# Kernel optimization log

Measured on AMD Instinct MI355X. Metric: run time of the kernel, lower is better.

Reference implementation:

```python
import jax, jax.numpy as jnp
import numpy as np

LN_EPS = 1e-5


def _ln(x, g, b):
    m = jnp.mean(x, axis=-1, keepdims=True)
    v = jnp.mean((x - m) ** 2, axis=-1, keepdims=True)
    return (x - m) / jnp.sqrt(v + LN_EPS) * g + b


def setup_inputs() -> dict:
    key = jax.random.key(0)
    ks = jax.random.split(key, 8)
    B, N, S, D, T = 16, 64, 2048, 1024, 768

    def xavier(k, shape):
        fan_in, fan_out = shape
        lim = (6.0 / (fan_in + fan_out)) ** 0.5
        return jax.random.uniform(k, shape, minval=-lim, maxval=lim, dtype=jnp.float32)

    return {
        "prev_states": jax.random.normal(ks[0], (B, N, D), dtype=jnp.float32),
        "input_tokens": jax.random.normal(ks[1], (B, S, T), dtype=jnp.float32),
        # input_projection (token_dim -> state_dim)
        "W_proj": xavier(ks[2], (T, D)),
        "b_proj": jnp.zeros((D,), jnp.float32),
        # three LayerNorms
        "g_state": jnp.ones((D,), jnp.float32), "beta_state": jnp.zeros((D,), jnp.float32),
        "g_input": jnp.ones((D,), jnp.float32), "beta_input": jnp.zeros((D,), jnp.float32),
        "g_out": jnp.ones((D,), jnp.float32), "beta_out": jnp.zeros((D,), jnp.float32),
        # GRU gates (2D -> D); update-gate bias initialized to -1 as in the module
        "W_u": xavier(ks[3], (2 * D, D)), "b_u": jnp.full((D,), -1.0, jnp.float32),
        "W_r": xavier(ks[4], (2 * D, D)), "b_r": jnp.zeros((D,), jnp.float32),
        "W_n": xavier(ks[5], (2 * D, D)), "b_n": jnp.zeros((D,), jnp.float32),
    }


def reference(prev_states, input_tokens, W_proj, b_proj,
              g_state, beta_state, g_input, beta_input, g_out, beta_out,
              W_u, b_u, W_r, b_r, W_n, b_n):
    D = prev_states.shape[-1]
    # project tokens to state dim: (B,S,D)
    tok = input_tokens @ W_proj + b_proj
    # attention routing (routing_weights=None path)
    scores = jnp.einsum('bnd,bsd->bns', prev_states, tok) / jnp.sqrt(jnp.float32(D))
    attn = jax.nn.softmax(scores, axis=-1)
    routed = jnp.einsum('bns,bsd->bnd', attn, tok)  # (B,N,D)
    # GRU-style gated update, vectorized over the num_states axis
    ps_n = _ln(prev_states, g_state, beta_state)
    in_n = _ln(routed, g_input, beta_input)
    concat = jnp.concatenate([ps_n, in_n], axis=-1)  # (B,N,2D)
    u = jax.nn.sigmoid(concat @ W_u + b_u)
    r = jax.nn.sigmoid(concat @ W_r + b_r)
    reset_in = jnp.concatenate([r * ps_n, in_n], axis=-1)
    cand = jnp.tanh(reset_in @ W_n + b_n)  # dropout is identity in eval
    new_state = (1.0 - u) * prev_states + u * cand
    return _ln(new_state, g_out, beta_out)
```

## Files before the change

kernel.cpp:

```cpp
#include <hip/hip_runtime.h>
#include <stdint.h>

typedef __attribute__((ext_vector_type(4))) float floatx4;
typedef __attribute__((ext_vector_type(8))) short shortx8;

#define LN_EPS 1e-5f

__device__ __forceinline__ unsigned short f2b(float f) {
  unsigned u = __builtin_bit_cast(unsigned, f);
  u = (u + 0x7FFFu + ((u >> 16) & 1u)) >> 16;
  return (unsigned short)u;
}
__device__ __forceinline__ float b2f(unsigned short h) {
  return __builtin_bit_cast(float, (unsigned)h << 16);
}

__device__ __forceinline__ void g2l16(const unsigned short* g, unsigned short* l) {
  __builtin_amdgcn_global_load_lds(
      (const __attribute__((address_space(1))) unsigned int*)g,
      (__attribute__((address_space(3))) unsigned int*)l, 16, 0, 0);
}

__device__ __forceinline__ float wave_sum(float v) {
#pragma unroll
  for (int o = 32; o; o >>= 1) v += __shfl_down(v, o, 64);
  return v;
}
__device__ __forceinline__ float block_sum(float v, float* s) {
  v = wave_sum(v);
  __syncthreads();
  if ((threadIdx.x & 63) == 0) s[threadIdx.x >> 6] = v;
  __syncthreads();
  return s[0] + s[1] + s[2] + s[3];
}

__global__ __launch_bounds__(256) void k_prep_pw(
    const float* __restrict__ prev, const float* __restrict__ wp,
    const float* __restrict__ Wu, const float* __restrict__ Wr,
    const float* __restrict__ Wn,
    unsigned short* __restrict__ Wtur, unsigned short* __restrict__ Wtn,
    unsigned short* __restrict__ Wtp, unsigned short* __restrict__ pwb,
    float* __restrict__ rs) {
  __shared__ unsigned short As[2][64 * 64];
  __shared__ unsigned short Bs[2][64 * 64];
  const int bid = blockIdx.x;
  const int tid = threadIdx.x;
  if (bid < 192) {
    const int wave = tid >> 6, lane = tid & 63;
    const int swz = (bid & 7) * 24 + (bid >> 3);
    const int m0 = (swz % 16) * 64;
    const int n0 = (swz / 16) * 64;
    const int wm = wave & 1, wn = wave >> 1;
    const int l16 = lane & 15, quad = lane >> 4;
    const int srow8 = lane >> 3;
    const int c8 = ((lane & 7) ^ srow8) * 8;

    const float* gAf[2];
    const float* gBf[2];
    int lOff[2];
#pragma unroll
    for (int j = 0; j < 2; j++) {
      const int rb = wave * 16 + j * 8;
      gAf[j] = prev + (long)(m0 + rb + srow8) * 1024 + c8;
      gBf[j] = wp + (long)(n0 + rb + srow8) * 1024 + c8;
      lOff[j] = rb * 64;
    }
    int offA[2][2], offB[2][2];
#pragma unroll
    for (int ks = 0; ks < 2; ks++)
#pragma unroll
      for (int i = 0; i < 2; i++) {
        int r = wm * 32 + i * 16 + l16;
        offA[ks][i] = r * 64 + (((ks * 4 + quad) ^ (r & 7)) * 8);
        r = wn * 32 + i * 16 + l16;
        offB[ks][i] = r * 64 + (((ks * 4 + quad) ^ (r & 7)) * 8);
      }

    floatx4 acc[2][2] = {};

#pragma unroll
    for (int j = 0; j < 2; j++) {
      floatx4 a0 = *(const floatx4*)(gAf[j]);
      floatx4 a1 = *(const floatx4*)(gAf[j] + 4);
      floatx4 b0 = *(const floatx4*)(gBf[j]);
      floatx4 b1 = *(const floatx4*)(gBf[j] + 4);
      unsigned short ta[8], tb[8];
#pragma unroll
      for (int i = 0; i < 4; i++) {
        ta[i] = f2b(a0[i]); ta[4 + i] = f2b(a1[i]);
        tb[i] = f2b(b0[i]); tb[4 + i] = f2b(b1[i]);
      }
      *(uint4*)&As[0][lOff[j] + lane * 8] = *(uint4*)ta;
      *(uint4*)&Bs[0][lOff[j] + lane * 8] = *(uint4*)tb;
    }
    __syncthreads();

    const int nt = 16;
    for (int t = 0; t < nt; t++) {
      const int cur = t & 1;
      floatx4 a0[2], a1[2], b0[2], b1[2];
      if (t + 1 < nt) {
        const int kn = (t + 1) << 6;
#pragma unroll
        for (int j = 0; j < 2; j++) {
          a0[j] = *(const floatx4*)(gAf[j] + kn);
          a1[j] = *(const floatx4*)(gAf[j] + kn + 4);
          b0[j] = *(const floatx4*)(gBf[j] + kn);
          b1[j] = *(const floatx4*)(gBf[j] + kn + 4);
        }
      }
#pragma unroll
      for (int ks = 0; ks < 2; ks++) {
        shortx8 af[2], bf[2];
#pragma unroll
        for (int i = 0; i < 2; i++) af[i] = *(const shortx8*)&As[cur][offA[ks][i]];
#pragma unroll
        for (int j = 0; j < 2; j++) bf[j] = *(const shortx8*)&Bs[cur][offB[ks][j]];
#pragma unroll
        for (int i = 0; i < 2; i++)
#pragma unroll
          for (int j = 0; j < 2; j++)
            acc[i][j] = __builtin_amdgcn_mfma_f32_16x16x32_bf16(af[i], bf[j], acc[i][j], 0, 0, 0);
      }
      if (t + 1 < nt) {
#pragma unroll
        for (int j = 0; j < 2; j++) {
          unsigned short ta[8], tb[8];
#pragma unroll
          for (int i = 0; i < 4; i++) {
            ta[i] = f2b(a0[j][i]); ta[4 + i] = f2b(a1[j][i]);
            tb[i] = f2b(b0[j][i]); tb[4 + i] = f2b(b1[j][i]);
          }
          *(uint4*)&As[cur ^ 1][lOff[j] + lane * 8] = *(uint4*)ta;
          *(uint4*)&Bs[cur ^ 1][lOff[j] + lane * 8] = *(uint4*)tb;
        }
      }
      __syncthreads();
    }

#pragma unroll
    for (int i = 0; i < 2; i++)
#pragma unroll
      for (int j = 0; j < 2; j++) {
        const int rbase = m0 + wm * 32 + i * 16 + quad * 4;
        const int c = n0 + wn * 32 + j * 16 + l16;
#pragma unroll
        for (int r = 0; r < 4; r++)
          pwb[(long)(rbase + r) * 768 + c] = f2b(acc[i][j][r]);
      }
    return;
  }
  float(*tile)[33] = (float(*)[33]) & As[0][0];
  if (bid == 192) {
    floatx4 z = {0.f, 0.f, 0.f, 0.f};
    *(floatx4*)(rs + tid * 4) = z;
  }
  int t = bid - 192;
  const float* in;
  unsigned short* out;
  int K, kx, ny;
  if (t < 6144) {
    const int which = t >> 11;
    const int t2 = t & 2047;
    kx = t2 & 63;
    ny = t2 >> 6;
    K = 2048;
    in = which == 0 ? Wu : (which == 1 ? Wr : Wn);
    out = which == 0 ? Wtur : (which == 1 ? Wtur + 1024 * 2048 : Wtn);
  } else {
    const int t2 = t - 6144;
    kx = t2 % 24;
    ny = t2 / 24;
    K = 768;
    in = wp;
    out = Wtp;
  }
  const int N = 1024;
  const int k0 = kx * 32, n0 = ny * 32;
  const int tx = tid & 31, ty = tid >> 5;
#pragma unroll
  for (int i = 0; i < 32; i += 8)
    tile[ty + i][tx] = in[(long)(k0 + ty + i) * N + n0 + tx];
  __syncthreads();
#pragma unroll
  for (int i = 0; i < 32; i += 8)
    out[(long)(n0 + ty + i) * K + k0 + tx] = f2b(tile[tx][ty + i]);
}

__global__ __launch_bounds__(256) void k_gemm64(
    const unsigned short* __restrict__ A, int lda,
    const unsigned short* __restrict__ Bt, int ldb,
    int K, long sCk,
    float* __restrict__ out, int ldc) {
  __shared__ unsigned short As[2][64 * 64];
  __shared__ unsigned short Bs[2][64 * 64];
  const int tid = threadIdx.x;
  const int wave = tid >> 6, lane = tid & 63;
  const int kc = blockIdx.z;
  const long koff = (long)kc * K;
  const int flat = blockIdx.x + blockIdx.y * gridDim.x;
  const int q = (gridDim.x * gridDim.y) >> 3;
  const int swz = (flat & 7) * q + (flat >> 3);
  const int m0 = (swz % gridDim.x) * 64;
  const int n0 = (swz / gridDim.x) * 64;
  const int wm = wave & 1, wn = wave >> 1;
  const int l16 = lane & 15, quad = lane >> 4;
  const int srow8 = lane >> 3;
  const int c8 = ((lane & 7) ^ srow8) * 8;

  const unsigned short* gA[2];
  const unsigned short* gB[2];
  int lOff[2];
#pragma unroll
  for (int j = 0; j < 2; j++) {
    const int rb = wave * 16 + j * 8;
    gA[j] = A + (long)(m0 + rb + srow8) * lda + c8 + koff;
    gB[j] = Bt + (long)(n0 + rb + srow8) * ldb + c8 + koff;
    lOff[j] = rb * 64;
  }
  int offA[2][2], offB[2][2];
#pragma unroll
  for (int ks = 0; ks < 2; ks++)
#pragma unroll
    for (int i = 0; i < 2; i++) {
      int r = wm * 32 + i * 16 + l16;
      offA[ks][i] = r * 64 + (((ks * 4 + quad) ^ (r & 7)) * 8);
      r = wn * 32 + i * 16 + l16;
      offB[ks][i] = r * 64 + (((ks * 4 + quad) ^ (r & 7)) * 8);
    }

  floatx4 acc[2][2] = {};

#pragma unroll
  for (int j = 0; j < 2; j++) {
    g2l16(gA[j], &As[0][lOff[j]]);
    g2l16(gB[j], &Bs[0][lOff[j]]);
  }
  __syncthreads();

  const int nt = K >> 6;
  for (int t = 0; t < nt; t++) {
    const int cur = t & 1;
    if (t + 1 < nt) {
      const int kn = (t + 1) << 6;
#pragma unroll
      for (int j = 0; j < 2; j++) {
        g2l16(gA[j] + kn, &As[cur ^ 1][lOff[j]]);
        g2l16(gB[j] + kn, &Bs[cur ^ 1][lOff[j]]);
      }
    }
#pragma unroll
    for (int ks = 0; ks < 2; ks++) {
      shortx8 af[2], bf[2];
#pragma unroll
      for (int i = 0; i < 2; i++) af[i] = *(const shortx8*)&As[cur][offA[ks][i]];
#pragma unroll
      for (int j = 0; j < 2; j++) bf[j] = *(const shortx8*)&Bs[cur][offB[ks][j]];
#pragma unroll
      for (int i = 0; i < 2; i++)
#pragma unroll
        for (int j = 0; j < 2; j++)
          acc[i][j] = __builtin_amdgcn_mfma_f32_16x16x32_bf16(af[i], bf[j], acc[i][j], 0, 0, 0);
    }
    __syncthreads();
  }

#pragma unroll
  for (int i = 0; i < 2; i++)
#pragma unroll
    for (int j = 0; j < 2; j++) {
      const int rbase = m0 + wm * 32 + i * 16 + quad * 4;
      const int c = n0 + wn * 32 + j * 16 + l16;
#pragma unroll
      for (int r = 0; r < 4; r++)
        out[(long)kc * sCk + (long)(rbase + r) * ldc + c] = acc[i][j][r];
    }
}

__global__ __launch_bounds__(256) void k_proj2_ln(
    const float* __restrict__ P0, int lda,
    const unsigned short* __restrict__ Bt, int ldb,
    int K,
    const float* __restrict__ bp, const float* __restrict__ rowsum,
    float* __restrict__ out, int ldc,
    const float* __restrict__ prev,
    const float* __restrict__ g_st, const float* __restrict__ be_st,
    unsigned short* __restrict__ conc) {
  __shared__ unsigned short As[2][64 * 64];
  __shared__ unsigned short Bs[2][64 * 64];
  const int tid = threadIdx.x;
  if (blockIdx.x >= 256) {
    float* scr = (float*)&As[0][0];
    const long r = blockIdx.x - 256;
    floatx4 v = *(const floatx4*)(prev + r * 1024 + tid * 4);
    float s1 = v[0] + v[1] + v[2] + v[3];
    float s2 = v[0] * v[0] + v[1] * v[1] + v[2] * v[2] + v[3] * v[3];
    s1 = block_sum(s1, scr);
    s2 = block_sum(s2, scr);
    const float mean = s1 * (1.0f / 1024.0f);
    const float var = s2 * (1.0f / 1024.0f) - mean * mean;
    const float rstd = rsqrtf(var + LN_EPS);
    unsigned short t4[4];
#pragma unroll
    for (int i = 0; i < 4; i++) {
      const int d = tid * 4 + i;
      t4[i] = f2b((v[i] - mean) * rstd * g_st[d] + be_st[d]);
    }
    *(uint2*)(conc + r * 2048 + tid * 4) = *(uint2*)t4;
    return;
  }
  const int wave = tid >> 6, lane = tid & 63;
  const int flat = blockIdx.x;
  const int swz = (flat & 7) * 32 + (flat >> 3);
  const int m0 = (swz % 16) * 64;
  const int n0 = (swz / 16) * 64;
  const int wm = wave & 1, wn = wave >> 1;
  const int l16 = lane & 15, quad = lane >> 4;
  const int srow8 = lane >> 3;
  const int c8 = ((lane & 7) ^ srow8) * 8;

  const float* gAf[2];
  const unsigned short* gB[2];
  int lOff[2];
#pragma unroll
  for (int j = 0; j < 2; j++) {
    const int rb = wave * 16 + j * 8;
    gAf[j] = P0 + (long)(m0 + rb + srow8) * lda + c8;
    gB[j] = Bt + (long)(n0 + rb + srow8) * ldb + c8;
    lOff[j] = rb * 64;
  }
  int offA[2][2], offB[2][2];
#pragma unroll
  for (int ks = 0; ks < 2; ks++)
#pragma unroll
    for (int i = 0; i < 2; i++) {
      int r = wm * 32 + i * 16 + l16;
      offA[ks][i] = r * 64 + (((ks * 4 + quad) ^ (r & 7)) * 8);
      r = wn * 32 + i * 16 + l16;
      offB[ks][i] = r * 64 + (((ks * 4 + quad) ^ (r & 7)) * 8);
    }

  floatx4 acc[2][2] = {};

#pragma unroll
  for (int j = 0; j < 2; j++) {
    g2l16(gB[j], &Bs[0][lOff[j]]);
    floatx4 a0 = *(const floatx4*)(gAf[j]);
    floatx4 a1 = *(const floatx4*)(gAf[j] + 4);
    floatx4 b0 = *(const floatx4*)(gAf[j] + 786432);
    floatx4 b1 = *(const floatx4*)(gAf[j] + 786432 + 4);
    unsigned short t8[8];
#pragma unroll
    for (int i = 0; i < 4; i++) { t8[i] = f2b(a0[i] + b0[i]); t8[4 + i] = f2b(a1[i] + b1[i]); }
    *(uint4*)&As[0][lOff[j] + lane * 8] = *(uint4*)t8;
  }
  __syncthreads();

  const int nt = K >> 6;
  for (int t = 0; t < nt; t++) {
    const int cur = t & 1;
    floatx4 a0[2], a1[2], p0[2], p1[2];
    if (t + 1 < nt) {
      const int kn = (t + 1) << 6;
#pragma unroll
      for (int j = 0; j < 2; j++) {
        g2l16(gB[j] + kn, &Bs[cur ^ 1][lOff[j]]);
        a0[j] = *(const floatx4*)(gAf[j] + kn);
        a1[j] = *(const floatx4*)(gAf[j] + kn + 4);
        p0[j] = *(const floatx4*)(gAf[j] + kn + 786432);
        p1[j] = *(const floatx4*)(gAf[j] + kn + 786432 + 4);
      }
    }
#pragma unroll
    for (int ks = 0; ks < 2; ks++) {
      shortx8 af[2], bf[2];
#pragma unroll
      for (int i = 0; i < 2; i++) af[i] = *(const shortx8*)&As[cur][offA[ks][i]];
#pragma unroll
      for (int j = 0; j < 2; j++) bf[j] = *(const shortx8*)&Bs[cur][offB[ks][j]];
#pragma unroll
      for (int i = 0; i < 2; i++)
#pragma unroll
        for (int j = 0; j < 2; j++)
          acc[i][j] = __builtin_amdgcn_mfma_f32_16x16x32_bf16(af[i], bf[j], acc[i][j], 0, 0, 0);
    }
    if (t + 1 < nt) {
#pragma unroll
      for (int j = 0; j < 2; j++) {
        unsigned short t8[8];
#pragma unroll
        for (int i = 0; i < 4; i++) {
          t8[i] = f2b(a0[j][i] + p0[j][i]);
          t8[4 + i] = f2b(a1[j][i] + p1[j][i]);
        }
        *(uint4*)&As[cur ^ 1][lOff[j] + lane * 8] = *(uint4*)t8;
      }
    }
    __syncthreads();
  }

#pragma unroll
  for (int i = 0; i < 2; i++)
#pragma unroll
    for (int j = 0; j < 2; j++) {
      const int rbase = m0 + wm * 32 + i * 16 + quad * 4;
      const int c = n0 + wn * 32 + j * 16 + l16;
#pragma unroll
      for (int r = 0; r < 4; r++) {
        const int row = rbase + r;
        out[(long)row * ldc + c] = acc[i][j][r] + rowsum[row] * bp[c];
      }
    }
}

__global__ __launch_bounds__(256) void k_scores(
    const unsigned short* __restrict__ A, long sAb, int lda,
    const float* __restrict__ toksf,
    int K, float scale,
    unsigned short* __restrict__ out2, int ldc, long sCb,
    float* __restrict__ rs) {
  __shared__ unsigned short As[2][64 * 64];
  __shared__ unsigned short Bs[2][64 * 64];
  const int tid = threadIdx.x;
  const int wave = tid >> 6, lane = tid & 63;
  const int b = blockIdx.z;
  const int m0 = 0, n0 = blockIdx.y * 64;
  const int wm = wave & 1, wn = wave >> 1;
  const int l16 = lane & 15, quad = lane >> 4;
  const int srow8 = lane >> 3;
  const int c8 = ((lane & 7) ^ srow8) * 8;
  const unsigned short* Ab = A + (long)b * sAb;

  const unsigned short* gA[2];
  const float* gBf[2];
  int lOff[2];
#pragma unroll
  for (int j = 0; j < 2; j++) {
    const int rb = wave * 16 + j * 8;
    gA[j] = Ab + (long)(m0 + rb + srow8) * lda + c8;
    gBf[j] = toksf + (long)b * 1572864 + (long)(n0 + rb + srow8) * 768 + c8;
    lOff[j] = rb * 64;
  }
  int offA[2][2], offB[2][2];
#pragma unroll
  for (int ks = 0; ks < 2; ks++)
#pragma unroll
    for (int i = 0; i < 2; i++) {
      int r = wm * 32 + i * 16 + l16;
      offA[ks][i] = r * 64 + (((ks * 4 + quad) ^ (r & 7)) * 8);
      r = wn * 32 + i * 16 + l16;
      offB[ks][i] = r * 64 + (((ks * 4 + quad) ^ (r & 7)) * 8);
    }

  floatx4 acc[2][2] = {};

#pragma unroll
  for (int j = 0; j < 2; j++) {
    g2l16(gA[j], &As[0][lOff[j]]);
    floatx4 v0 = *(const floatx4*)(gBf[j]);
    floatx4 v1 = *(const floatx4*)(gBf[j] + 4);
    unsigned short t8[8];
#pragma unroll
    for (int i = 0; i < 4; i++) { t8[i] = f2b(v0[i]); t8[4 + i] = f2b(v1[i]); }
    *(uint4*)&Bs[0][lOff[j] + lane * 8] = *(uint4*)t8;
  }
  __syncthreads();

  const int nt = K >> 6;
  for (int t = 0; t < nt; t++) {
    const int cur = t & 1;
    floatx4 w0[2], w1[2];
    if (t + 1 < nt) {
      const int kn = (t + 1) << 6;
#pragma unroll
      for (int j = 0; j < 2; j++) {
        g2l16(gA[j] + kn, &As[cur ^ 1][lOff[j]]);
        w0[j] = *(const floatx4*)(gBf[j] + kn);
        w1[j] = *(const floatx4*)(gBf[j] + kn + 4);
      }
    }
#pragma unroll
    for (int ks = 0; ks < 2; ks++) {
      shortx8 af[2], bf[2];
#pragma unroll
      for (int i = 0; i < 2; i++) af[i] = *(const shortx8*)&As[cur][offA[ks][i]];
#pragma unroll
      for (int j = 0; j < 2; j++) bf[j] = *(const shortx8*)&Bs[cur][offB[ks][j]];
#pragma unroll
      for (int i = 0; i < 2; i++)
#pragma unroll
        for (int j = 0; j < 2; j++)
          acc[i][j] = __builtin_amdgcn_mfma_f32_16x16x32_bf16(af[i], bf[j], acc[i][j], 0, 0, 0);
    }
    if (t + 1 < nt) {
#pragma unroll
      for (int j = 0; j < 2; j++) {
        unsigned short t8[8];
#pragma unroll
        for (int i = 0; i < 4; i++) { t8[i] = f2b(w0[j][i]); t8[4 + i] = f2b(w1[j][i]); }
        *(uint4*)&Bs[cur ^ 1][lOff[j] + lane * 8] = *(uint4*)t8;
      }
    }
    __syncthreads();
  }

#pragma unroll
  for (int i = 0; i < 2; i++) {
    float psum[4] = {0.f, 0.f, 0.f, 0.f};
#pragma unroll
    for (int j = 0; j < 2; j++) {
      const int rbase = m0 + wm * 32 + i * 16 + quad * 4;
      const int c = n0 + wn * 32 + j * 16 + l16;
#pragma unroll
      for (int r = 0; r < 4; r++) {
        const float e = expf(acc[i][j][r] * scale);
        out2[(long)b * sCb + (long)(rbase + r) * ldc + c] = f2b(e);
        psum[r] += e;
      }
    }
#pragma unroll
    for (int r = 0; r < 4; r++) {
      float s = psum[r];
      s += __shfl_xor(s, 1, 64);
      s += __shfl_xor(s, 2, 64);
      s += __shfl_xor(s, 4, 64);
      s += __shfl_xor(s, 8, 64);
      if (l16 == 0)
        atomicAdd(rs + (long)b * 64 + m0 + wm * 32 + i * 16 + quad * 4 + r, s);
    }
  }
}

__global__ __launch_bounds__(256) void k_routed_mfma(
    const unsigned short* __restrict__ attnb,
    const float* __restrict__ tokf,
    float* __restrict__ parts) {
  __shared__ unsigned short As[64 * 40];
  __shared__ unsigned short Bs[32 * 66];
  const int kc = blockIdx.x, nt = blockIdx.y, b = blockIdx.z;
  const int tid = threadIdx.x;
  const int wave = tid >> 6, lane = tid & 63;
  const int wm = wave & 1, wn = wave >> 1;
  const int l16 = lane & 15, quad = lane >> 4;
  const int n0 = nt * 64;
  const long abase = (long)b * 131072 + (long)kc * 1024;
  const long tbase = ((long)b * 2048 + (long)kc * 1024) * 768;
  const int srow = tid >> 2, skc = (tid & 3) * 8;
  const int bk = tid >> 3, bd = (tid & 7) * 8;

  floatx4 acc[2][2] = {};

  uint4 pa = *(const uint4*)(attnb + abase + (long)srow * 2048 + skc);
  floatx4 f0 = *(const floatx4*)(tokf + tbase + (long)bk * 768 + n0 + bd);
  floatx4 f1 = *(const floatx4*)(tokf + tbase + (long)bk * 768 + n0 + bd + 4);

  for (int k0 = 0; k0 < 1024; k0 += 32) {
    *(uint4*)&As[srow * 40 + skc] = pa;
    {
      unsigned short t8[8];
#pragma unroll
      for (int i = 0; i < 4; i++) { t8[i] = f2b(f0[i]); t8[4 + i] = f2b(f1[i]); }
      unsigned short* dst = &Bs[bk * 66 + bd];
#pragma unroll
      for (int w2 = 0; w2 < 4; w2++) *(unsigned*)(dst + w2 * 2) = ((unsigned*)t8)[w2];
    }
    if (k0 + 32 < 1024) {
      pa = *(const uint4*)(attnb + abase + (long)srow * 2048 + (k0 + 32) + skc);
      f0 = *(const floatx4*)(tokf + tbase + (long)(k0 + 32 + bk) * 768 + n0 + bd);
      f1 = *(const floatx4*)(tokf + tbase + (long)(k0 + 32 + bk) * 768 + n0 + bd + 4);
    }
    asm volatile("s_waitcnt lgkmcnt(0)" ::: "memory");
    __builtin_amdgcn_s_barrier();
    __builtin_amdgcn_sched_barrier(0);

    shortx8 a0 = *(const shortx8*)&As[(wm * 32 + 0  + l16) * 40 + quad * 8];
    shortx8 a1 = *(const shortx8*)&As[(wm * 32 + 16 + l16) * 40 + quad * 8];
    shortx8 b0, b1;
#pragma unroll
    for (int j = 0; j < 8; j++) {
      b0[j] = *(const short*)&Bs[(quad * 8 + j) * 66 + wn * 32 + l16];
      b1[j] = *(const short*)&Bs[(quad * 8 + j) * 66 + wn * 32 + 16 + l16];
    }
    acc[0][0] = __builtin_amdgcn_mfma_f32_16x16x32_bf16(a0, b0, acc[0][0], 0, 0, 0);
    acc[0][1] = __builtin_amdgcn_mfma_f32_16x16x32_bf16(a0, b1, acc[0][1], 0, 0, 0);
    acc[1][0] = __builtin_amdgcn_mfma_f32_16x16x32_bf16(a1, b0, acc[1][0], 0, 0, 0);
    acc[1][1] = __builtin_amdgcn_mfma_f32_16x16x32_bf16(a1, b1, acc[1][1], 0, 0, 0);
    __builtin_amdgcn_s_barrier();
  }

#pragma unroll
  for (int im = 0; im < 2; im++)
#pragma unroll
    for (int in_ = 0; in_ < 2; in_++) {
      const int rbase = wm * 32 + im * 16 + quad * 4;
      const int c = n0 + wn * 32 + in_ * 16 + l16;
#pragma unroll
      for (int r = 0; r < 4; r++)
        parts[(long)kc * 786432 + ((long)b * 64 + rbase + r) * 768 + c] =
            acc[im][in_][r];
    }
}

__global__ __launch_bounds__(256) void k_ln_routed(
    const float* __restrict__ routed,
    const float* __restrict__ g_in, const float* __restrict__ be_in,
    unsigned short* __restrict__ conc, unsigned short* __restrict__ candA) {
  __shared__ float scr[4];
  const long r = blockIdx.x;
  const int t = threadIdx.x;
  floatx4 v = *(const floatx4*)(routed + r * 1024 + t * 4);
  float s1 = v[0] + v[1] + v[2] + v[3];
  float s2 = v[0] * v[0] + v[1] * v[1] + v[2] * v[2] + v[3] * v[3];
  s1 = block_sum(s1, scr);
  s2 = block_sum(s2, scr);
  const float mean = s1 * (1.0f / 1024.0f);
  const float var = s2 * (1.0f / 1024.0f) - mean * mean;
  const float rstd = rsqrtf(var + LN_EPS);
  unsigned short t4[4];
#pragma unroll
  for (int i = 0; i < 4; i++) {
    const int d = t * 4 + i;
    t4[i] = f2b((v[i] - mean) * rstd * g_in[d] + be_in[d]);
  }
  *(uint2*)(conc + r * 2048 + 1024 + t * 4) = *(uint2*)t4;
  *(uint2*)(candA + r * 2048 + 1024 + t * 4) = *(uint2*)t4;
}

__global__ __launch_bounds__(256) void k_gate_epi(
    const float* __restrict__ gparts,
    const float* __restrict__ bu, const float* __restrict__ br,
    const unsigned short* __restrict__ conc,
    float* __restrict__ ubuf, unsigned short* __restrict__ candA) {
  const int row = blockIdx.x >> 1;
  const int half = blockIdx.x & 1;
  const int t = threadIdx.x;
  const long base = (long)row * 2048 + half * 1024 + t * 4;
  floatx4 p0 = *(const floatx4*)(gparts + base);
  floatx4 p1 = *(const floatx4*)(gparts + 2097152 + base);
  const float* bias = half ? br : bu;
  floatx4 bv = *(const floatx4*)(bias + t * 4);
  if (!half) {
    floatx4 o;
#pragma unroll
    for (int i = 0; i < 4; i++)
      o[i] = 1.0f / (1.0f + expf(-(p0[i] + p1[i] + bv[i])));
    *(floatx4*)(ubuf + (long)row * 1024 + t * 4) = o;
  } else {
    unsigned short t4[4];
#pragma unroll
    for (int i = 0; i < 4; i++) {
      float rr = 1.0f / (1.0f + expf(-(p0[i] + p1[i] + bv[i])));
      t4[i] = f2b(rr * b2f(conc[(long)row * 2048 + t * 4 + i]));
    }
    *(uint2*)(candA + (long)row * 2048 + t * 4) = *(uint2*)t4;
  }
}

__global__ __launch_bounds__(256) void k_ln_out(
    const float* __restrict__ cparts,
    const float* __restrict__ ubuf, const float* __restrict__ prev,
    const float* __restrict__ bn,
    const float* __restrict__ g, const float* __restrict__ be,
    float* __restrict__ out) {
  __shared__ float scr[4];
  const long r = blockIdx.x;
  const int t = threadIdx.x;
  floatx4 p0 = *(const floatx4*)(cparts + r * 1024 + t * 4);
  floatx4 p1 = *(const floatx4*)(cparts + 1048576 + r * 1024 + t * 4);
  floatx4 uu = *(const floatx4*)(ubuf + r * 1024 + t * 4);
  floatx4 pv = *(const floatx4*)(prev + r * 1024 + t * 4);
  floatx4 bv = *(const floatx4*)(bn + t * 4);
  floatx4 v;
#pragma unroll
  for (int i = 0; i < 4; i++) {
    const float cand = tanhf(p0[i] + p1[i] + bv[i]);
    v[i] = (1.0f - uu[i]) * pv[i] + uu[i] * cand;
  }
  float s1 = v[0] + v[1] + v[2] + v[3];
  float s2 = v[0] * v[0] + v[1] * v[1] + v[2] * v[2] + v[3] * v[3];
  s1 = block_sum(s1, scr);
  s2 = block_sum(s2, scr);
  const float mean = s1 * (1.0f / 1024.0f);
  const float var = s2 * (1.0f / 1024.0f) - mean * mean;
  const float rstd = rsqrtf(var + LN_EPS);
  floatx4 o;
#pragma unroll
  for (int i = 0; i < 4; i++) {
    const int d = t * 4 + i;
    o[i] = (v[i] - mean) * rstd * g[d] + be[d];
  }
  *(floatx4*)(out + r * 1024 + t * 4) = o;
}

extern "C" void kernel_launch(void* const* d_in, const int* in_sizes, int n_in,
                              void* d_out, int out_size, void* d_ws, size_t ws_size,
                              hipStream_t stream) {
  (void)in_sizes; (void)n_in; (void)out_size; (void)ws_size;
  const float* prev  = (const float*)d_in[0];
  const float* toks  = (const float*)d_in[1];
  const float* Wp    = (const float*)d_in[2];
  const float* bp    = (const float*)d_in[3];
  const float* g_st  = (const float*)d_in[4];
  const float* be_st = (const float*)d_in[5];
  const float* g_in  = (const float*)d_in[6];
  const float* be_in = (const float*)d_in[7];
  const float* g_o   = (const float*)d_in[8];
  const float* be_o  = (const float*)d_in[9];
  const float* Wu    = (const float*)d_in[10];
  const float* bu    = (const float*)d_in[11];
  const float* Wr    = (const float*)d_in[12];
  const float* br    = (const float*)d_in[13];
  const float* Wn    = (const float*)d_in[14];
  const float* bn    = (const float*)d_in[15];
  float* out = (float*)d_out;

  char* ws = (char*)d_ws;
  unsigned short* Wtp   = (unsigned short*)ws; ws += 1572864;
  unsigned short* pwb   = (unsigned short*)ws; ws += 1572864;
  unsigned short* attnb = (unsigned short*)ws; ws += 4194304;
  float*          rowsum= (float*)ws;          ws += 4096;
  float*          parts = (float*)ws;          ws += 6291456;
  float*          routed= (float*)ws;          ws += 4194304;
  unsigned short* conc  = (unsigned short*)ws; ws += 4194304;
  unsigned short* candA = (unsigned short*)ws; ws += 4194304;
  float*          ubuf  = (float*)ws;          ws += 4194304;
  unsigned short* Wtur  = (unsigned short*)ws; ws += 8388608;
  unsigned short* Wtn   = (unsigned short*)ws; ws += 4194304;
  float*          gparts= (float*)ws;          ws += 16777216;
  float*          cparts= (float*)ws;          ws += 8388608;

  const dim3 blk(256);

  k_prep_pw<<<dim3(7104), blk, 0, stream>>>(prev, Wp, Wu, Wr, Wn,
                                            Wtur, Wtn, Wtp, pwb, rowsum);
  k_scores<<<dim3(1, 32, 16), blk, 0, stream>>>(
      pwb, 49152L, 768, toks, 768, 0.03125f,
      attnb, 2048, 131072L, rowsum);
  k_routed_mfma<<<dim3(2, 12, 16), blk, 0, stream>>>(attnb, toks, parts);
  k_proj2_ln<<<dim3(1280), blk, 0, stream>>>(
      parts, 768, Wtp, 768, 768, bp, rowsum, routed, 1024,
      prev, g_st, be_st, conc);
  k_ln_routed<<<dim3(1024), blk, 0, stream>>>(routed, g_in, be_in, conc, candA);
  k_gemm64<<<dim3(16, 32, 2), blk, 0, stream>>>(
      conc, 2048, Wtur, 2048, 1024, 2097152L, gparts, 2048);
  k_gate_epi<<<dim3(2048), blk, 0, stream>>>(gparts, bu, br, conc, ubuf, candA);
  k_gemm64<<<dim3(16, 16, 2), blk, 0, stream>>>(
      candA, 2048, Wtn, 2048, 1024, 1048576L, cparts, 1024);
  k_ln_out<<<dim3(1024), blk, 0, stream>>>(cparts, ubuf, prev, bn, g_o, be_o, out);
}
```

Baseline: 294.8 us.

## Fuse LayerNorm and gate epilogues into GEMM A-operand loaders

Removes the separate routed-LayerNorm and gate-epilogue kernels. The projection GEMM epilogue now accumulates per-row sum and sum-of-squares with atomics. The gate GEMMs build their bf16 A tiles on the fly: normalized routed values for one K-half, and sigmoid(r)*ps_n for the candidate GEMM. The update gate sigmoid is recomputed in the final LayerNorm kernel, which drops the conc, candA and ubuf buffers and two launches. The cost is extra ALU work and fp32 global loads inside the GEMM main loops, plus atomic contention on the row statistics.

```diff
diff --git a/kernel.cpp b/kernel.cpp
--- a/kernel.cpp
+++ b/kernel.cpp
@@ -14,6 +14,7 @@
 __device__ __forceinline__ float b2f(unsigned short h) {
   return __builtin_bit_cast(float, (unsigned)h << 16);
 }
+__device__ __forceinline__ float sigm(float x) { return 1.0f / (1.0f + expf(-x)); }
 
 __device__ __forceinline__ void g2l16(const unsigned short* g, unsigned short* l) {
   __builtin_amdgcn_global_load_lds(
@@ -40,7 +41,7 @@
     const float* __restrict__ Wn,
     unsigned short* __restrict__ Wtur, unsigned short* __restrict__ Wtn,
     unsigned short* __restrict__ Wtp, unsigned short* __restrict__ pwb,
-    float* __restrict__ rs) {
+    float* __restrict__ rs, float* __restrict__ rstat) {
   __shared__ unsigned short As[2][64 * 64];
   __shared__ unsigned short Bs[2][64 * 64];
   const int bid = blockIdx.x;
@@ -154,6 +155,11 @@
   if (bid == 192) {
     floatx4 z = {0.f, 0.f, 0.f, 0.f};
     *(floatx4*)(rs + tid * 4) = z;
+  }
+  if (bid == 193) {
+    floatx4 z = {0.f, 0.f, 0.f, 0.f};
+    *(floatx4*)(rstat + tid * 8) = z;
+    *(floatx4*)(rstat + tid * 8 + 4) = z;
   }
   int t = bid - 192;
   const float* in;
@@ -187,232 +193,6 @@
     out[(long)(n0 + ty + i) * K + k0 + tx] = f2b(tile[tx][ty + i]);
 }
 
-__global__ __launch_bounds__(256) void k_gemm64(
-    const unsigned short* __restrict__ A, int lda,
-    const unsigned short* __restrict__ Bt, int ldb,
-    int K, long sCk,
-    float* __restrict__ out, int ldc) {
-  __shared__ unsigned short As[2][64 * 64];
-  __shared__ unsigned short Bs[2][64 * 64];
-  const int tid = threadIdx.x;
-  const int wave = tid >> 6, lane = tid & 63;
-  const int kc = blockIdx.z;
-  const long koff = (long)kc * K;
-  const int flat = blockIdx.x + blockIdx.y * gridDim.x;
-  const int q = (gridDim.x * gridDim.y) >> 3;
-  const int swz = (flat & 7) * q + (flat >> 3);
-  const int m0 = (swz % gridDim.x) * 64;
-  const int n0 = (swz / gridDim.x) * 64;
-  const int wm = wave & 1, wn = wave >> 1;
-  const int l16 = lane & 15, quad = lane >> 4;
-  const int srow8 = lane >> 3;
-  const int c8 = ((lane & 7) ^ srow8) * 8;
-
-  const unsigned short* gA[2];
-  const unsigned short* gB[2];
-  int lOff[2];
-#pragma unroll
-  for (int j = 0; j < 2; j++) {
-    const int rb = wave * 16 + j * 8;
-    gA[j] = A + (long)(m0 + rb + srow8) * lda + c8 + koff;
-    gB[j] = Bt + (long)(n0 + rb + srow8) * ldb + c8 + koff;
-    lOff[j] = rb * 64;
-  }
-  int offA[2][2], offB[2][2];
-#pragma unroll
-  for (int ks = 0; ks < 2; ks++)
-#pragma unroll
-    for (int i = 0; i < 2; i++) {
-      int r = wm * 32 + i * 16 + l16;
-      offA[ks][i] = r * 64 + (((ks * 4 + quad) ^ (r & 7)) * 8);
-      r = wn * 32 + i * 16 + l16;
-      offB[ks][i] = r * 64 + (((ks * 4 + quad) ^ (r & 7)) * 8);
-    }
-
-  floatx4 acc[2][2] = {};
-
-#pragma unroll
-  for (int j = 0; j < 2; j++) {
-    g2l16(gA[j], &As[0][lOff[j]]);
-    g2l16(gB[j], &Bs[0][lOff[j]]);
-  }
-  __syncthreads();
-
-  const int nt = K >> 6;
-  for (int t = 0; t < nt; t++) {
-    const int cur = t & 1;
-    if (t + 1 < nt) {
-      const int kn = (t + 1) << 6;
-#pragma unroll
-      for (int j = 0; j < 2; j++) {
-        g2l16(gA[j] + kn, &As[cur ^ 1][lOff[j]]);
-        g2l16(gB[j] + kn, &Bs[cur ^ 1][lOff[j]]);
-      }
-    }
-#pragma unroll
-    for (int ks = 0; ks < 2; ks++) {
-      shortx8 af[2], bf[2];
-#pragma unroll
-      for (int i = 0; i < 2; i++) af[i] = *(const shortx8*)&As[cur][offA[ks][i]];
-#pragma unroll
-      for (int j = 0; j < 2; j++) bf[j] = *(const shortx8*)&Bs[cur][offB[ks][j]];
-#pragma unroll
-      for (int i = 0; i < 2; i++)
-#pragma unroll
-        for (int j = 0; j < 2; j++)
-          acc[i][j] = __builtin_amdgcn_mfma_f32_16x16x32_bf16(af[i], bf[j], acc[i][j], 0, 0, 0);
-    }
-    __syncthreads();
-  }
-
-#pragma unroll
-  for (int i = 0; i < 2; i++)
-#pragma unroll
-    for (int j = 0; j < 2; j++) {
-      const int rbase = m0 + wm * 32 + i * 16 + quad * 4;
-      const int c = n0 + wn * 32 + j * 16 + l16;
-#pragma unroll
-      for (int r = 0; r < 4; r++)
-        out[(long)kc * sCk + (long)(rbase + r) * ldc + c] = acc[i][j][r];
-    }
-}
-
-__global__ __launch_bounds__(256) void k_proj2_ln(
-    const float* __restrict__ P0, int lda,
-    const unsigned short* __restrict__ Bt, int ldb,
-    int K,
-    const float* __restrict__ bp, const float* __restrict__ rowsum,
-    float* __restrict__ out, int ldc,
-    const float* __restrict__ prev,
-    const float* __restrict__ g_st, const float* __restrict__ be_st,
-    unsigned short* __restrict__ conc) {
-  __shared__ unsigned short As[2][64 * 64];
-  __shared__ unsigned short Bs[2][64 * 64];
-  const int tid = threadIdx.x;
-  if (blockIdx.x >= 256) {
-    float* scr = (float*)&As[0][0];
-    const long r = blockIdx.x - 256;
-    floatx4 v = *(const floatx4*)(prev + r * 1024 + tid * 4);
-    float s1 = v[0] + v[1] + v[2] + v[3];
-    float s2 = v[0] * v[0] + v[1] * v[1] + v[2] * v[2] + v[3] * v[3];
-    s1 = block_sum(s1, scr);
-    s2 = block_sum(s2, scr);
-    const float mean = s1 * (1.0f / 1024.0f);
-    const float var = s2 * (1.0f / 1024.0f) - mean * mean;
-    const float rstd = rsqrtf(var + LN_EPS);
-    unsigned short t4[4];
-#pragma unroll
-    for (int i = 0; i < 4; i++) {
-      const int d = tid * 4 + i;
-      t4[i] = f2b((v[i] - mean) * rstd * g_st[d] + be_st[d]);
-    }
-    *(uint2*)(conc + r * 2048 + tid * 4) = *(uint2*)t4;
-    return;
-  }
-  const int wave = tid >> 6, lane = tid & 63;
-  const int flat = blockIdx.x;
-  const int swz = (flat & 7) * 32 + (flat >> 3);
-  const int m0 = (swz % 16) * 64;
-  const int n0 = (swz / 16) * 64;
-  const int wm = wave & 1, wn = wave >> 1;
-  const int l16 = lane & 15, quad = lane >> 4;
-  const int srow8 = lane >> 3;
-  const int c8 = ((lane & 7) ^ srow8) * 8;
-
-  const float* gAf[2];
-  const unsigned short* gB[2];
-  int lOff[2];
-#pragma unroll
-  for (int j = 0; j < 2; j++) {
-    const int rb = wave * 16 + j * 8;
-    gAf[j] = P0 + (long)(m0 + rb + srow8) * lda + c8;
-    gB[j] = Bt + (long)(n0 + rb + srow8) * ldb + c8;
-    lOff[j] = rb * 64;
-  }
-  int offA[2][2], offB[2][2];
-#pragma unroll
-  for (int ks = 0; ks < 2; ks++)
-#pragma unroll
-    for (int i = 0; i < 2; i++) {
-      int r = wm * 32 + i * 16 + l16;
-      offA[ks][i] = r * 64 + (((ks * 4 + quad) ^ (r & 7)) * 8);
-      r = wn * 32 + i * 16 + l16;
-      offB[ks][i] = r * 64 + (((ks * 4 + quad) ^ (r & 7)) * 8);
-    }
-
-  floatx4 acc[2][2] = {};
-
-#pragma unroll
-  for (int j = 0; j < 2; j++) {
-    g2l16(gB[j], &Bs[0][lOff[j]]);
-    floatx4 a0 = *(const floatx4*)(gAf[j]);
-    floatx4 a1 = *(const floatx4*)(gAf[j] + 4);
-    floatx4 b0 = *(const floatx4*)(gAf[j] + 786432);
-    floatx4 b1 = *(const floatx4*)(gAf[j] + 786432 + 4);
-    unsigned short t8[8];
-#pragma unroll
-    for (int i = 0; i < 4; i++) { t8[i] = f2b(a0[i] + b0[i]); t8[4 + i] = f2b(a1[i] + b1[i]); }
-    *(uint4*)&As[0][lOff[j] + lane * 8] = *(uint4*)t8;
-  }
-  __syncthreads();
-
-  const int nt = K >> 6;
-  for (int t = 0; t < nt; t++) {
-    const int cur = t & 1;
-    floatx4 a0[2], a1[2], p0[2], p1[2];
-    if (t + 1 < nt) {
-      const int kn = (t + 1) << 6;
-#pragma unroll
-      for (int j = 0; j < 2; j++) {
-        g2l16(gB[j] + kn, &Bs[cur ^ 1][lOff[j]]);
-        a0[j] = *(const floatx4*)(gAf[j] + kn);
-        a1[j] = *(const floatx4*)(gAf[j] + kn + 4);
-        p0[j] = *(const floatx4*)(gAf[j] + kn + 786432);
-        p1[j] = *(const floatx4*)(gAf[j] + kn + 786432 + 4);
-      }
-    }
-#pragma unroll
-    for (int ks = 0; ks < 2; ks++) {
-      shortx8 af[2], bf[2];
-#pragma unroll
-      for (int i = 0; i < 2; i++) af[i] = *(const shortx8*)&As[cur][offA[ks][i]];
-#pragma unroll
-      for (int j = 0; j < 2; j++) bf[j] = *(const shortx8*)&Bs[cur][offB[ks][j]];
-#pragma unroll
-      for (int i = 0; i < 2; i++)
-#pragma unroll
-        for (int j = 0; j < 2; j++)
-          acc[i][j] = __builtin_amdgcn_mfma_f32_16x16x32_bf16(af[i], bf[j], acc[i][j], 0, 0, 0);
-    }
-    if (t + 1 < nt) {
-#pragma unroll
-      for (int j = 0; j < 2; j++) {
-        unsigned short t8[8];
-#pragma unroll
-        for (int i = 0; i < 4; i++) {
-          t8[i] = f2b(a0[j][i] + p0[j][i]);
-          t8[4 + i] = f2b(a1[j][i] + p1[j][i]);
-        }
-        *(uint4*)&As[cur ^ 1][lOff[j] + lane * 8] = *(uint4*)t8;
-      }
-    }
-    __syncthreads();
-  }
-
-#pragma unroll
-  for (int i = 0; i < 2; i++)
-#pragma unroll
-    for (int j = 0; j < 2; j++) {
-      const int rbase = m0 + wm * 32 + i * 16 + quad * 4;
-      const int c = n0 + wn * 32 + j * 16 + l16;
-#pragma unroll
-      for (int r = 0; r < 4; r++) {
-        const int row = rbase + r;
-        out[(long)row * ldc + c] = acc[i][j][r] + rowsum[row] * bp[c];
-      }
-    }
-}
-
 __global__ __launch_bounds__(256) void k_scores(
     const unsigned short* __restrict__ A, long sAb, int lda,
     const float* __restrict__ toksf,
@@ -601,64 +381,359 @@
     }
 }
 
-__global__ __launch_bounds__(256) void k_ln_routed(
-    const float* __restrict__ routed,
+__global__ __launch_bounds__(256) void k_proj2_ln(
+    const float* __restrict__ P0, int lda,
+    const unsigned short* __restrict__ Bt, int ldb,
+    int K,
+    const float* __restrict__ bp, const float* __restrict__ rowsum,
+    float* __restrict__ out, int ldc, float* __restrict__ rstat,
+    const float* __restrict__ prev,
+    const float* __restrict__ g_st, const float* __restrict__ be_st,
+    unsigned short* __restrict__ psn) {
+  __shared__ unsigned short As[2][64 * 64];
+  __shared__ unsigned short Bs[2][64 * 64];
+  const int tid = threadIdx.x;
+  if (blockIdx.x >= 256) {
+    float* scr = (float*)&As[0][0];
+    const long r = blockIdx.x - 256;
+    floatx4 v = *(const floatx4*)(prev + r * 1024 + tid * 4);
+    float s1 = v[0] + v[1] + v[2] + v[3];
+    float s2 = v[0] * v[0] + v[1] * v[1] + v[2] * v[2] + v[3] * v[3];
+    s1 = block_sum(s1, scr);
+    s2 = block_sum(s2, scr);
+    const float mean = s1 * (1.0f / 1024.0f);
+    const float var = s2 * (1.0f / 1024.0f) - mean * mean;
+    const float rstd = rsqrtf(var + LN_EPS);
+    unsigned short t4[4];
+#pragma unroll
+    for (int i = 0; i < 4; i++) {
+      const int d = tid * 4 + i;
+      t4[i] = f2b((v[i] - mean) * rstd * g_st[d] + be_st[d]);
+    }
+    *(uint2*)(psn + r * 1024 + tid * 4) = *(uint2*)t4;
+    return;
+  }
+  const int wave = tid >> 6, lane = tid & 63;
+  const int flat = blockIdx.x;
+  const int swz = (flat & 7) * 32 + (flat >> 3);
+  const int m0 = (swz % 16) * 64;
+  const int n0 = (swz / 16) * 64;
+  const int wm = wave & 1, wn = wave >> 1;
+  const int l16 = lane & 15, quad = lane >> 4;
+  const int srow8 = lane >> 3;
+  const int c8 = ((lane & 7) ^ srow8) * 8;
+
+  const float* gAf[2];
+  const unsigned short* gB[2];
+  int lOff[2];
+#pragma unroll
+  for (int j = 0; j < 2; j++) {
+    const int rb = wave * 16 + j * 8;
+    gAf[j] = P0 + (long)(m0 + rb + srow8) * lda + c8;
+    gB[j] = Bt + (long)(n0 + rb + srow8) * ldb + c8;
+    lOff[j] = rb * 64;
+  }
+  int offA[2][2], offB[2][2];
+#pragma unroll
+  for (int ks = 0; ks < 2; ks++)
+#pragma unroll
+    for (int i = 0; i < 2; i++) {
+      int r = wm * 32 + i * 16 + l16;
+      offA[ks][i] = r * 64 + (((ks * 4 + quad) ^ (r & 7)) * 8);
+      r = wn * 32 + i * 16 + l16;
+      offB[ks][i] = r * 64 + (((ks * 4 + quad) ^ (r & 7)) * 8);
+    }
+
+  floatx4 acc[2][2] = {};
+
+#pragma unroll
+  for (int j = 0; j < 2; j++) {
+    g2l16(gB[j], &Bs[0][lOff[j]]);
+    floatx4 a0 = *(const floatx4*)(gAf[j]);
+    floatx4 a1 = *(const floatx4*)(gAf[j] + 4);
+    floatx4 b0 = *(const floatx4*)(gAf[j] + 786432);
+    floatx4 b1 = *(const floatx4*)(gAf[j] + 786432 + 4);
+    unsigned short t8[8];
+#pragma unroll
+    for (int i = 0; i < 4; i++) { t8[i] = f2b(a0[i] + b0[i]); t8[4 + i] = f2b(a1[i] + b1[i]); }
+    *(uint4*)&As[0][lOff[j] + lane * 8] = *(uint4*)t8;
+  }
+  __syncthreads();
+
+  const int nt = K >> 6;
+  for (int t = 0; t < nt; t++) {
+    const int cur = t & 1;
+    floatx4 a0[2], a1[2], p0[2], p1[2];
+    if (t + 1 < nt) {
+      const int kn = (t + 1) << 6;
+#pragma unroll
+      for (int j = 0; j < 2; j++) {
+        g2l16(gB[j] + kn, &Bs[cur ^ 1][lOff[j]]);
+        a0[j] = *(const floatx4*)(gAf[j] + kn);
+        a1[j] = *(const floatx4*)(gAf[j] + kn + 4);
+        p0[j] = *(const floatx4*)(gAf[j] + kn + 786432);
+        p1[j] = *(const floatx4*)(gAf[j] + kn + 786432 + 4);
+      }
+    }
+#pragma unroll
+    for (int ks = 0; ks < 2; ks++) {
+      shortx8 af[2], bf[2];
+#pragma unroll
+      for (int i = 0; i < 2; i++) af[i] = *(const shortx8*)&As[cur][offA[ks][i]];
+#pragma unroll
+      for (int j = 0; j < 2; j++) bf[j] = *(const shortx8*)&Bs[cur][offB[ks][j]];
+#pragma unroll
+      for (int i = 0; i < 2; i++)
+#pragma unroll
+        for (int j = 0; j < 2; j++)
+          acc[i][j] = __builtin_amdgcn_mfma_f32_16x16x32_bf16(af[i], bf[j], acc[i][j], 0, 0, 0);
+    }
+    if (t + 1 < nt) {
+#pragma unroll
+      for (int j = 0; j < 2; j++) {
+        unsigned short t8[8];
+#pragma unroll
+        for (int i = 0; i < 4; i++) {
+          t8[i] = f2b(a0[j][i] + p0[j][i]);
+          t8[4 + i] = f2b(a1[j][i] + p1[j][i]);
+        }
+        *(uint4*)&As[cur ^ 1][lOff[j] + lane * 8] = *(uint4*)t8;
+      }
+    }
+    __syncthreads();
+  }
+
+#pragma unroll
+  for (int i = 0; i < 2; i++) {
+    float s1[4] = {0.f, 0.f, 0.f, 0.f};
+    float s2[4] = {0.f, 0.f, 0.f, 0.f};
+    const int rbase = m0 + wm * 32 + i * 16 + quad * 4;
+#pragma unroll
+    for (int j = 0; j < 2; j++) {
+      const int c = n0 + wn * 32 + j * 16 + l16;
+#pragma unroll
+      for (int r = 0; r < 4; r++) {
+        const int row = rbase + r;
+        float v = acc[i][j][r] + rowsum[row] * bp[c];
+        out[(long)row * ldc + c] = v;
+        s1[r] += v;
+        s2[r] += v * v;
+      }
+    }
+#pragma unroll
+    for (int r = 0; r < 4; r++) {
+      float a = s1[r], b = s2[r];
+      a += __shfl_xor(a, 1, 64); b += __shfl_xor(b, 1, 64);
+      a += __shfl_xor(a, 2, 64); b += __shfl_xor(b, 2, 64);
+      a += __shfl_xor(a, 4, 64); b += __shfl_xor(b, 4, 64);
+      a += __shfl_xor(a, 8, 64); b += __shfl_xor(b, 8, 64);
+      if (l16 == 0) {
+        atomicAdd(rstat + (rbase + r) * 2, a);
+        atomicAdd(rstat + (rbase + r) * 2 + 1, b);
+      }
+    }
+  }
+}
+
+__global__ __launch_bounds__(256) void k_gemm2(
+    const unsigned short* __restrict__ Abf, int lda,
+    const float* __restrict__ routed, const float* __restrict__ rstat,
     const float* __restrict__ g_in, const float* __restrict__ be_in,
-    unsigned short* __restrict__ conc, unsigned short* __restrict__ candA) {
-  __shared__ float scr[4];
-  const long r = blockIdx.x;
-  const int t = threadIdx.x;
-  floatx4 v = *(const floatx4*)(routed + r * 1024 + t * 4);
-  float s1 = v[0] + v[1] + v[2] + v[3];
-  float s2 = v[0] * v[0] + v[1] * v[1] + v[2] * v[2] + v[3] * v[3];
-  s1 = block_sum(s1, scr);
-  s2 = block_sum(s2, scr);
-  const float mean = s1 * (1.0f / 1024.0f);
-  const float var = s2 * (1.0f / 1024.0f) - mean * mean;
-  const float rstd = rsqrtf(var + LN_EPS);
-  unsigned short t4[4];
-#pragma unroll
-  for (int i = 0; i < 4; i++) {
-    const int d = t * 4 + i;
-    t4[i] = f2b((v[i] - mean) * rstd * g_in[d] + be_in[d]);
-  }
-  *(uint2*)(conc + r * 2048 + 1024 + t * 4) = *(uint2*)t4;
-  *(uint2*)(candA + r * 2048 + 1024 + t * 4) = *(uint2*)t4;
-}
-
-__global__ __launch_bounds__(256) void k_gate_epi(
-    const float* __restrict__ gparts,
-    const float* __restrict__ bu, const float* __restrict__ br,
-    const unsigned short* __restrict__ conc,
-    float* __restrict__ ubuf, unsigned short* __restrict__ candA) {
-  const int row = blockIdx.x >> 1;
-  const int half = blockIdx.x & 1;
-  const int t = threadIdx.x;
-  const long base = (long)row * 2048 + half * 1024 + t * 4;
-  floatx4 p0 = *(const floatx4*)(gparts + base);
-  floatx4 p1 = *(const floatx4*)(gparts + 2097152 + base);
-  const float* bias = half ? br : bu;
-  floatx4 bv = *(const floatx4*)(bias + t * 4);
-  if (!half) {
-    floatx4 o;
-#pragma unroll
-    for (int i = 0; i < 4; i++)
-      o[i] = 1.0f / (1.0f + expf(-(p0[i] + p1[i] + bv[i])));
-    *(floatx4*)(ubuf + (long)row * 1024 + t * 4) = o;
+    const float* __restrict__ gparts, const float* __restrict__ br,
+    const unsigned short* __restrict__ psn,
+    const unsigned short* __restrict__ Bt, int ldb,
+    int K, long sCk, int amode0, int amode1,
+    float* __restrict__ out, int ldc) {
+  __shared__ unsigned short As[2][64 * 64];
+  __shared__ unsigned short Bs[2][64 * 64];
+  const int tid = threadIdx.x;
+  const int wave = tid >> 6, lane = tid & 63;
+  const int kc = blockIdx.z;
+  const int amode = kc == 0 ? amode0 : amode1;
+  const long koff = (long)kc * K;
+  const int flat = blockIdx.x + blockIdx.y * gridDim.x;
+  const int q = (gridDim.x * gridDim.y) >> 3;
+  const int swz = (flat & 7) * q + (flat >> 3);
+  const int m0 = (swz % gridDim.x) * 64;
+  const int n0 = (swz / gridDim.x) * 64;
+  const int wm = wave & 1, wn = wave >> 1;
+  const int l16 = lane & 15, quad = lane >> 4;
+  const int srow8 = lane >> 3;
+  const int c8 = ((lane & 7) ^ srow8) * 8;
+
+  int arow[2];
+  const unsigned short* gA[2];
+  const unsigned short* gB[2];
+  int lOff[2];
+  float mean_[2], rstd_[2];
+#pragma unroll
+  for (int j = 0; j < 2; j++) {
+    const int rb = wave * 16 + j * 8;
+    arow[j] = m0 + rb + srow8;
+    gA[j] = Abf ? Abf + (long)arow[j] * lda + c8 : nullptr;
+    gB[j] = Bt + (long)(n0 + rb + srow8) * ldb + c8 + koff;
+    lOff[j] = rb * 64;
+    if (amode == 1) {
+      const float s1 = rstat[arow[j] * 2];
+      const float s2 = rstat[arow[j] * 2 + 1];
+      const float mean = s1 * (1.0f / 1024.0f);
+      const float var = s2 * (1.0f / 1024.0f) - mean * mean;
+      mean_[j] = mean;
+      rstd_[j] = rsqrtf(var + LN_EPS);
+    }
+  }
+  int offA[2][2], offB[2][2];
+#pragma unroll
+  for (int ks = 0; ks < 2; ks++)
+#pragma unroll
+    for (int i = 0; i < 2; i++) {
+      int r = wm * 32 + i * 16 + l16;
+      offA[ks][i] = r * 64 + (((ks * 4 + quad) ^ (r & 7)) * 8);
+      r = wn * 32 + i * 16 + l16;
+      offB[ks][i] = r * 64 + (((ks * 4 + quad) ^ (r & 7)) * 8);
+    }
+
+  floatx4 acc[2][2] = {};
+
+#pragma unroll
+  for (int j = 0; j < 2; j++) g2l16(gB[j], &Bs[0][lOff[j]]);
+  if (amode == 0) {
+#pragma unroll
+    for (int j = 0; j < 2; j++) g2l16(gA[j], &As[0][lOff[j]]);
+  } else if (amode == 1) {
+#pragma unroll
+    for (int j = 0; j < 2; j++) {
+      floatx4 v0 = *(const floatx4*)(routed + (long)arow[j] * 1024 + c8);
+      floatx4 v1 = *(const floatx4*)(routed + (long)arow[j] * 1024 + c8 + 4);
+      floatx4 gg0 = *(const floatx4*)(g_in + c8);
+      floatx4 gg1 = *(const floatx4*)(g_in + c8 + 4);
+      floatx4 bb0 = *(const floatx4*)(be_in + c8);
+      floatx4 bb1 = *(const floatx4*)(be_in + c8 + 4);
+      unsigned short t8[8];
+#pragma unroll
+      for (int i = 0; i < 4; i++) {
+        t8[i] = f2b((v0[i] - mean_[j]) * rstd_[j] * gg0[i] + bb0[i]);
+        t8[4 + i] = f2b((v1[i] - mean_[j]) * rstd_[j] * gg1[i] + bb1[i]);
+      }
+      *(uint4*)&As[0][lOff[j] + lane * 8] = *(uint4*)t8;
+    }
   } else {
-    unsigned short t4[4];
-#pragma unroll
-    for (int i = 0; i < 4; i++) {
-      float rr = 1.0f / (1.0f + expf(-(p0[i] + p1[i] + bv[i])));
-      t4[i] = f2b(rr * b2f(conc[(long)row * 2048 + t * 4 + i]));
-    }
-    *(uint2*)(candA + (long)row * 2048 + t * 4) = *(uint2*)t4;
-  }
+#pragma unroll
+    for (int j = 0; j < 2; j++) {
+      const long gbase = (long)arow[j] * 2048 + 1024 + c8;
+      floatx4 q0 = *(const floatx4*)(gparts + gbase);
+      floatx4 q1 = *(const floatx4*)(gparts + gbase + 4);
+      floatx4 q2 = *(const floatx4*)(gparts + 2097152 + gbase);
+      floatx4 q3 = *(const floatx4*)(gparts + 2097152 + gbase + 4);
+      floatx4 bb0 = *(const floatx4*)(br + c8);
+      floatx4 bb1 = *(const floatx4*)(br + c8 + 4);
+      uint4 pv = *(const uint4*)(psn + (long)arow[j] * 1024 + c8);
+      const unsigned short* ph = (const unsigned short*)&pv;
+      unsigned short t8[8];
+#pragma unroll
+      for (int i = 0; i < 4; i++) {
+        t8[i] = f2b(sigm(q0[i] + q2[i] + bb0[i]) * b2f(ph[i]));
+        t8[4 + i] = f2b(sigm(q1[i] + q3[i] + bb1[i]) * b2f(ph[4 + i]));
+      }
+      *(uint4*)&As[0][lOff[j] + lane * 8] = *(uint4*)t8;
+    }
+  }
+  __syncthreads();
+
+  const int nt = K >> 6;
+  for (int t = 0; t < nt; t++) {
+    const int cur = t & 1;
+    const int kn = (t + 1) << 6;
+    floatx4 rv0[2], rv1[2], q0[2], q1[2], q2[2], q3[2];
+    uint4 pv[2];
+    if (t + 1 < nt) {
+#pragma unroll
+      for (int j = 0; j < 2; j++) g2l16(gB[j] + kn, &Bs[cur ^ 1][lOff[j]]);
+      if (amode == 0) {
+#pragma unroll
+        for (int j = 0; j < 2; j++) g2l16(gA[j] + kn, &As[cur ^ 1][lOff[j]]);
+      } else if (amode == 1) {
+#pragma unroll
+        for (int j = 0; j < 2; j++) {
+          rv0[j] = *(const floatx4*)(routed + (long)arow[j] * 1024 + kn + c8);
+          rv1[j] = *(const floatx4*)(routed + (long)arow[j] * 1024 + kn + c8 + 4);
+        }
+      } else {
+#pragma unroll
+        for (int j = 0; j < 2; j++) {
+          const long gbase = (long)arow[j] * 2048 + 1024 + kn + c8;
+          q0[j] = *(const floatx4*)(gparts + gbase);
+          q1[j] = *(const floatx4*)(gparts + gbase + 4);
+          q2[j] = *(const floatx4*)(gparts + 2097152 + gbase);
+          q3[j] = *(const floatx4*)(gparts + 2097152 + gbase + 4);
+          pv[j] = *(const uint4*)(psn + (long)arow[j] * 1024 + kn + c8);
+        }
+      }
+    }
+#pragma unroll
+    for (int ks = 0; ks < 2; ks++) {
+      shortx8 af[2], bf[2];
+#pragma unroll
+      for (int i = 0; i < 2; i++) af[i] = *(const shortx8*)&As[cur][offA[ks][i]];
+#pragma unroll
+      for (int j = 0; j < 2; j++) bf[j] = *(const shortx8*)&Bs[cur][offB[ks][j]];
+#pragma unroll
+      for (int i = 0; i < 2; i++)
+#pragma unroll
+        for (int j = 0; j < 2; j++)
+          acc[i][j] = __builtin_amdgcn_mfma_f32_16x16x32_bf16(af[i], bf[j], acc[i][j], 0, 0, 0);
+    }
+    if (t + 1 < nt) {
+      if (amode == 1) {
+#pragma unroll
+        for (int j = 0; j < 2; j++) {
+          floatx4 gg0 = *(const floatx4*)(g_in + kn + c8);
+          floatx4 gg1 = *(const floatx4*)(g_in + kn + c8 + 4);
+          floatx4 bb0 = *(const floatx4*)(be_in + kn + c8);
+          floatx4 bb1 = *(const floatx4*)(be_in + kn + c8 + 4);
+          unsigned short t8[8];
+#pragma unroll
+          for (int i = 0; i < 4; i++) {
+            t8[i] = f2b((rv0[j][i] - mean_[j]) * rstd_[j] * gg0[i] + bb0[i]);
+            t8[4 + i] = f2b((rv1[j][i] - mean_[j]) * rstd_[j] * gg1[i] + bb1[i]);
+          }
+          *(uint4*)&As[cur ^ 1][lOff[j] + lane * 8] = *(uint4*)t8;
+        }
+      } else if (amode == 2) {
+#pragma unroll
+        for (int j = 0; j < 2; j++) {
+          floatx4 bb0 = *(const floatx4*)(br + kn + c8);
+          floatx4 bb1 = *(const floatx4*)(br + kn + c8 + 4);
+          const unsigned short* ph = (const unsigned short*)&pv[j];
+          unsigned short t8[8];
+#pragma unroll
+          for (int i = 0; i < 4; i++) {
+            t8[i] = f2b(sigm(q0[j][i] + q2[j][i] + bb0[i]) * b2f(ph[i]));
+            t8[4 + i] = f2b(sigm(q1[j][i] + q3[j][i] + bb1[i]) * b2f(ph[4 + i]));
+          }
+          *(uint4*)&As[cur ^ 1][lOff[j] + lane * 8] = *(uint4*)t8;
+        }
+      }
+    }
+    __syncthreads();
+  }
+
+#pragma unroll
+  for (int i = 0; i < 2; i++)
+#pragma unroll
+    for (int j = 0; j < 2; j++) {
+      const int rbase = m0 + wm * 32 + i * 16 + quad * 4;
+      const int c = n0 + wn * 32 + j * 16 + l16;
+#pragma unroll
+      for (int r = 0; r < 4; r++)
+        out[(long)kc * sCk + (long)(rbase + r) * ldc + c] = acc[i][j][r];
+    }
 }
 
 __global__ __launch_bounds__(256) void k_ln_out(
     const float* __restrict__ cparts,
-    const float* __restrict__ ubuf, const float* __restrict__ prev,
+    const float* __restrict__ gparts,
+    const float* __restrict__ bu, const float* __restrict__ prev,
     const float* __restrict__ bn,
     const float* __restrict__ g, const float* __restrict__ be,
     float* __restrict__ out) {
@@ -667,14 +742,17 @@
   const int t = threadIdx.x;
   floatx4 p0 = *(const floatx4*)(cparts + r * 1024 + t * 4);
   floatx4 p1 = *(const floatx4*)(cparts + 1048576 + r * 1024 + t * 4);
-  floatx4 uu = *(const floatx4*)(ubuf + r * 1024 + t * 4);
+  floatx4 u0 = *(const floatx4*)(gparts + r * 2048 + t * 4);
+  floatx4 u1 = *(const floatx4*)(gparts + 2097152 + r * 2048 + t * 4);
+  floatx4 ub = *(const floatx4*)(bu + t * 4);
   floatx4 pv = *(const floatx4*)(prev + r * 1024 + t * 4);
   floatx4 bv = *(const floatx4*)(bn + t * 4);
   floatx4 v;
 #pragma unroll
   for (int i = 0; i < 4; i++) {
+    const float uu = sigm(u0[i] + u1[i] + ub[i]);
     const float cand = tanhf(p0[i] + p1[i] + bv[i]);
-    v[i] = (1.0f - uu[i]) * pv[i] + uu[i] * cand;
+    v[i] = (1.0f - uu) * pv[i] + uu * cand;
   }
   float s1 = v[0] + v[1] + v[2] + v[3];
   float s2 = v[0] * v[0] + v[1] * v[1] + v[2] * v[2] + v[3] * v[3];
@@ -719,11 +797,10 @@
   unsigned short* pwb   = (unsigned short*)ws; ws += 1572864;
   unsigned short* attnb = (unsigned short*)ws; ws += 4194304;
   float*          rowsum= (float*)ws;          ws += 4096;
+  float*          rstat = (float*)ws;          ws += 8192;
   float*          parts = (float*)ws;          ws += 6291456;
   float*          routed= (float*)ws;          ws += 4194304;
-  unsigned short* conc  = (unsigned short*)ws; ws += 4194304;
-  unsigned short* candA = (unsigned short*)ws; ws += 4194304;
-  float*          ubuf  = (float*)ws;          ws += 4194304;
+  unsigned short* psn   = (unsigned short*)ws; ws += 2097152;
   unsigned short* Wtur  = (unsigned short*)ws; ws += 8388608;
   unsigned short* Wtn   = (unsigned short*)ws; ws += 4194304;
   float*          gparts= (float*)ws;          ws += 16777216;
@@ -732,19 +809,20 @@
   const dim3 blk(256);
 
   k_prep_pw<<<dim3(7104), blk, 0, stream>>>(prev, Wp, Wu, Wr, Wn,
-                                            Wtur, Wtn, Wtp, pwb, rowsum);
+                                            Wtur, Wtn, Wtp, pwb, rowsum, rstat);
   k_scores<<<dim3(1, 32, 16), blk, 0, stream>>>(
       pwb, 49152L, 768, toks, 768, 0.03125f,
       attnb, 2048, 131072L, rowsum);
   k_routed_mfma<<<dim3(2, 12, 16), blk, 0, stream>>>(attnb, toks, parts);
   k_proj2_ln<<<dim3(1280), blk, 0, stream>>>(
-      parts, 768, Wtp, 768, 768, bp, rowsum, routed, 1024,
-      prev, g_st, be_st, conc);
-  k_ln_routed<<<dim3(1024), blk, 0, stream>>>(routed, g_in, be_in, conc, candA);
-  k_gemm64<<<dim3(16, 32, 2), blk, 0, stream>>>(
-      conc, 2048, Wtur, 2048, 1024, 2097152L, gparts, 2048);
-  k_gate_epi<<<dim3(2048), blk, 0, stream>>>(gparts, bu, br, conc, ubuf, candA);
-  k_gemm64<<<dim3(16, 16, 2), blk, 0, stream>>>(
-      candA, 2048, Wtn, 2048, 1024, 1048576L, cparts, 1024);
-  k_ln_out<<<dim3(1024), blk, 0, stream>>>(cparts, ubuf, prev, bn, g_o, be_o, out);
-}
+      parts, 768, Wtp, 768, 768, bp, rowsum, routed, 1024, rstat,
+      prev, g_st, be_st, psn);
+  k_gemm2<<<dim3(16, 32, 2), blk, 0, stream>>>(
+      psn, 1024, routed, rstat, g_in, be_in, nullptr, nullptr, nullptr,
+      Wtur, 2048, 1024, 2097152L, 0, 1, gparts, 2048);
+  k_gemm2<<<dim3(16, 16, 2), blk, 0, stream>>>(
+      nullptr, 0, routed, rstat, g_in, be_in, gparts, br, psn,
+      Wtn, 2048, 1024, 1048576L, 2, 1, cparts, 1024);
+  k_ln_out<<<dim3(1024), blk, 0, stream>>>(cparts, gparts, bu, prev, bn,
+                                           g_o, be_o, out);
+}
```

Result: slower. 345.4 us (+17.2%).
